# Performance work log

Measured on AMD Instinct MI355X. Metric: run time of the kernel, lower is better.

Reference implementation:

```python
import jax, jax.numpy as jnp
import numpy as np


def setup_inputs() -> dict:
    key = jax.random.key(0)
    k1, k2, k3 = jax.random.split(key, 3)
    B, N = 1024, 32768
    inputs = jax.random.normal(k1, (B, N), dtype=jnp.float32)
    targets = jax.random.randint(k2, (B,), 0, 16384, dtype=jnp.int64)
    postive_list = jax.random.randint(k3, (B,), 0, 64, dtype=jnp.int64)
    return {"inputs": inputs, "targets": targets, "postive_list": postive_list}


def reference(inputs, targets, postive_list):
    # log_softmax over the candidate axis
    logsm = jax.nn.log_softmax(inputs, axis=1)  # [B, N]
    N = inputs.shape[1]
    pos = jnp.arange(N)  # [N]
    start = targets[:, None]                      # [B, 1]
    end = (targets + postive_list)[:, None]       # inclusive end, [B, 1]
    mask = (pos[None, :] >= start) & (pos[None, :] <= end)  # [B, N]
    # per-sample mean of -log_softmax over the ragged range (length = postive+1)
    count = (postive_list + 1).astype(inputs.dtype)  # [B]
    per_sample = -jnp.sum(jnp.where(mask, logsm, 0.0), axis=1) / count  # [B]
    return jnp.mean(per_sample)
```

## Files before the change

kernel.cpp:

```cpp
#include <hip/hip_runtime.h>
#include <math.h>

#define THREADS 256
#define WAVES (THREADS / 64)

__global__ __launch_bounds__(THREADS)
void ce_loss_kernel(const float* __restrict__ x,
                    const int* __restrict__ targets,
                    const int* __restrict__ positives,
                    float* __restrict__ out,
                    int N, float invB)
{
    const int b = blockIdx.x;
    const float4* row4 = reinterpret_cast<const float4*>(x + (size_t)b * N);
    const int t0 = targets[b];
    const int t1 = t0 + positives[b];
    const int n4 = N >> 2;

    float m = -INFINITY;
    float s = 0.0f;
    float wsum = 0.0f;

    for (int i = threadIdx.x; i < n4; i += THREADS) {
        float4 v = row4[i];
        const int j = i << 2;

        float vm = fmaxf(fmaxf(v.x, v.y), fmaxf(v.z, v.w));
        if (vm > m) { s *= __expf(m - vm); m = vm; }
        s += __expf(v.x - m);
        s += __expf(v.y - m);
        s += __expf(v.z - m);
        s += __expf(v.w - m);

        wsum += (j     >= t0 && j     <= t1) ? v.x : 0.0f;
        wsum += (j + 1 >= t0 && j + 1 <= t1) ? v.y : 0.0f;
        wsum += (j + 2 >= t0 && j + 2 <= t1) ? v.z : 0.0f;
        wsum += (j + 3 >= t0 && j + 3 <= t1) ? v.w : 0.0f;
    }

    #pragma unroll
    for (int off = 32; off > 0; off >>= 1) {
        float om = __shfl_xor(m, off, 64);
        float os = __shfl_xor(s, off, 64);
        float ow = __shfl_xor(wsum, off, 64);
        float nm = fmaxf(m, om);
        s = s * __expf(m - nm) + os * __expf(om - nm);
        m = nm;
        wsum += ow;
    }

    __shared__ float sm[WAVES], ss[WAVES], sw[WAVES];
    const int wave = threadIdx.x >> 6;
    const int lane = threadIdx.x & 63;
    if (lane == 0) { sm[wave] = m; ss[wave] = s; sw[wave] = wsum; }
    __syncthreads();

    if (threadIdx.x == 0) {
        m = sm[0]; s = ss[0]; wsum = sw[0];
        #pragma unroll
        for (int w = 1; w < WAVES; ++w) {
            float om = sm[w], os = ss[w];
            float nm = fmaxf(m, om);
            s = s * __expf(m - nm) + os * __expf(om - nm);
            m = nm;
            wsum += sw[w];
        }
        const float count = (float)(t1 - t0 + 1);
        const float per_sample = (m + logf(s)) - wsum / count;
        atomicAdd(out, per_sample * invB);
    }
}

extern "C" void kernel_launch(void* const* d_in, const int* in_sizes, int n_in,
                              void* d_out, int out_size, void* d_ws, size_t ws_size,
                              hipStream_t stream) {
    const float* inputs    = (const float*)d_in[0];
    const int*   targets   = (const int*)d_in[1];
    const int*   positives = (const int*)d_in[2];
    float* out = (float*)d_out;

    const int B = in_sizes[1];
    const int N = in_sizes[0] / B;

    hipMemsetAsync(d_out, 0, sizeof(float), stream);

    ce_loss_kernel<<<B, THREADS, 0, stream>>>(inputs, targets, positives, out,
                                              N, 1.0f / (float)B);
}
```

Measured before the change: 201.9 us.

## Use multiple independent online-LSE accumulators, wider blocks, and two-stage final reduction

Each thread now keeps eight independent running max/sum pairs and processes two float4 loads per iteration, with 512 threads per block. This is meant to break the serial exp dependency chain and raise memory-level parallelism. The window check becomes a single unsigned compare. The atomic accumulation and memset are replaced by per-row results in the workspace plus a small reduction kernel. The per-element update now evaluates two exps instead of roughly one, and adds a second kernel launch.

```diff
diff --git a/kernel.cpp b/kernel.cpp
--- a/kernel.cpp
+++ b/kernel.cpp
@@ -1,74 +1,122 @@
 #include <hip/hip_runtime.h>
 #include <math.h>
 
-#define THREADS 256
+#define THREADS 512
 #define WAVES (THREADS / 64)
 
+#define LSE_UPD(mk, sk, v)                                    \
+    {                                                         \
+        float nm_ = fmaxf((mk), (v));                         \
+        (sk) = (sk) * __expf((mk) - nm_) + __expf((v) - nm_); \
+        (mk) = nm_;                                           \
+    }
+
+#define LSE_MERGE(ma, sa, mb, sb)                                  \
+    {                                                              \
+        float nm_ = fmaxf((ma), (mb));                             \
+        (sa) = (sa) * __expf((ma) - nm_) + (sb) * __expf((mb) - nm_); \
+        (ma) = nm_;                                                \
+    }
+
 __global__ __launch_bounds__(THREADS)
-void ce_loss_kernel(const float* __restrict__ x,
-                    const int* __restrict__ targets,
-                    const int* __restrict__ positives,
-                    float* __restrict__ out,
-                    int N, float invB)
+void ce_row_kernel(const float* __restrict__ x,
+                   const int* __restrict__ targets,
+                   const int* __restrict__ positives,
+                   float* __restrict__ row_out,
+                   int N)
 {
     const int b = blockIdx.x;
     const float4* row4 = reinterpret_cast<const float4*>(x + (size_t)b * N);
     const int t0 = targets[b];
-    const int t1 = t0 + positives[b];
+    const unsigned wlen = (unsigned)positives[b];
     const int n4 = N >> 2;
 
-    float m = -INFINITY;
-    float s = 0.0f;
-    float wsum = 0.0f;
+    float m0 = -INFINITY, m1 = -INFINITY, m2 = -INFINITY, m3 = -INFINITY;
+    float m4 = -INFINITY, m5 = -INFINITY, m6 = -INFINITY, m7 = -INFINITY;
+    float s0 = 0.f, s1 = 0.f, s2 = 0.f, s3 = 0.f;
+    float s4 = 0.f, s5 = 0.f, s6 = 0.f, s7 = 0.f;
+    float wsum = 0.f;
 
-    for (int i = threadIdx.x; i < n4; i += THREADS) {
-        float4 v = row4[i];
-        const int j = i << 2;
+    int i = threadIdx.x;
+    for (; i + THREADS < n4; i += 2 * THREADS) {
+        float4 a = row4[i];
+        float4 c = row4[i + THREADS];
+        const int ja = i << 2;
+        const int jc = (i + THREADS) << 2;
 
-        float vm = fmaxf(fmaxf(v.x, v.y), fmaxf(v.z, v.w));
-        if (vm > m) { s *= __expf(m - vm); m = vm; }
-        s += __expf(v.x - m);
-        s += __expf(v.y - m);
-        s += __expf(v.z - m);
-        s += __expf(v.w - m);
+        LSE_UPD(m0, s0, a.x); LSE_UPD(m1, s1, a.y);
+        LSE_UPD(m2, s2, a.z); LSE_UPD(m3, s3, a.w);
+        LSE_UPD(m4, s4, c.x); LSE_UPD(m5, s5, c.y);
+        LSE_UPD(m6, s6, c.z); LSE_UPD(m7, s7, c.w);
 
-        wsum += (j     >= t0 && j     <= t1) ? v.x : 0.0f;
-        wsum += (j + 1 >= t0 && j + 1 <= t1) ? v.y : 0.0f;
-        wsum += (j + 2 >= t0 && j + 2 <= t1) ? v.z : 0.0f;
-        wsum += (j + 3 >= t0 && j + 3 <= t1) ? v.w : 0.0f;
+        wsum += ((unsigned)(ja     - t0) <= wlen) ? a.x : 0.f;
+        wsum += ((unsigned)(ja + 1 - t0) <= wlen) ? a.y : 0.f;
+        wsum += ((unsigned)(ja + 2 - t0) <= wlen) ? a.z : 0.f;
+        wsum += ((unsigned)(ja + 3 - t0) <= wlen) ? a.w : 0.f;
+        wsum += ((unsigned)(jc     - t0) <= wlen) ? c.x : 0.f;
+        wsum += ((unsigned)(jc + 1 - t0) <= wlen) ? c.y : 0.f;
+        wsum += ((unsigned)(jc + 2 - t0) <= wlen) ? c.z : 0.f;
+        wsum += ((unsigned)(jc + 3 - t0) <= wlen) ? c.w : 0.f;
     }
+    if (i < n4) {
+        float4 a = row4[i];
+        const int ja = i << 2;
+        LSE_UPD(m0, s0, a.x); LSE_UPD(m1, s1, a.y);
+        LSE_UPD(m2, s2, a.z); LSE_UPD(m3, s3, a.w);
+        wsum += ((unsigned)(ja     - t0) <= wlen) ? a.x : 0.f;
+        wsum += ((unsigned)(ja + 1 - t0) <= wlen) ? a.y : 0.f;
+        wsum += ((unsigned)(ja + 2 - t0) <= wlen) ? a.z : 0.f;
+        wsum += ((unsigned)(ja + 3 - t0) <= wlen) ? a.w : 0.f;
+    }
+
+    LSE_MERGE(m0, s0, m1, s1); LSE_MERGE(m2, s2, m3, s3);
+    LSE_MERGE(m4, s4, m5, s5); LSE_MERGE(m6, s6, m7, s7);
+    LSE_MERGE(m0, s0, m2, s2); LSE_MERGE(m4, s4, m6, s6);
+    LSE_MERGE(m0, s0, m4, s4);
 
     #pragma unroll
     for (int off = 32; off > 0; off >>= 1) {
-        float om = __shfl_xor(m, off, 64);
-        float os = __shfl_xor(s, off, 64);
+        float om = __shfl_xor(m0, off, 64);
+        float os = __shfl_xor(s0, off, 64);
         float ow = __shfl_xor(wsum, off, 64);
-        float nm = fmaxf(m, om);
-        s = s * __expf(m - nm) + os * __expf(om - nm);
-        m = nm;
+        LSE_MERGE(m0, s0, om, os);
         wsum += ow;
     }
 
     __shared__ float sm[WAVES], ss[WAVES], sw[WAVES];
     const int wave = threadIdx.x >> 6;
     const int lane = threadIdx.x & 63;
-    if (lane == 0) { sm[wave] = m; ss[wave] = s; sw[wave] = wsum; }
+    if (lane == 0) { sm[wave] = m0; ss[wave] = s0; sw[wave] = wsum; }
     __syncthreads();
 
     if (threadIdx.x == 0) {
-        m = sm[0]; s = ss[0]; wsum = sw[0];
+        m0 = sm[0]; s0 = ss[0]; wsum = sw[0];
         #pragma unroll
         for (int w = 1; w < WAVES; ++w) {
-            float om = sm[w], os = ss[w];
-            float nm = fmaxf(m, om);
-            s = s * __expf(m - nm) + os * __expf(om - nm);
-            m = nm;
+            LSE_MERGE(m0, s0, sm[w], ss[w]);
             wsum += sw[w];
         }
-        const float count = (float)(t1 - t0 + 1);
-        const float per_sample = (m + logf(s)) - wsum / count;
-        atomicAdd(out, per_sample * invB);
+        const float count = (float)(wlen + 1u);
+        row_out[b] = (m0 + logf(s0)) - wsum / count;
     }
+}
+
+__global__ __launch_bounds__(256)
+void ce_reduce_kernel(const float* __restrict__ row_vals,
+                      float* __restrict__ out, int B, float invB)
+{
+    float acc = 0.f;
+    for (int i = threadIdx.x; i < B; i += 256) acc += row_vals[i];
+    #pragma unroll
+    for (int off = 32; off > 0; off >>= 1) acc += __shfl_xor(acc, off, 64);
+
+    __shared__ float sb[4];
+    const int wave = threadIdx.x >> 6;
+    const int lane = threadIdx.x & 63;
+    if (lane == 0) sb[wave] = acc;
+    __syncthreads();
+    if (threadIdx.x == 0)
+        out[0] = (sb[0] + sb[1] + sb[2] + sb[3]) * invB;
 }
 
 extern "C" void kernel_launch(void* const* d_in, const int* in_sizes, int n_in,
@@ -78,12 +126,12 @@
     const int*   targets   = (const int*)d_in[1];
     const int*   positives = (const int*)d_in[2];
     float* out = (float*)d_out;
+    float* row_vals = (float*)d_ws;
 
     const int B = in_sizes[1];
     const int N = in_sizes[0] / B;
 
-    hipMemsetAsync(d_out, 0, sizeof(float), stream);
-
-    ce_loss_kernel<<<B, THREADS, 0, stream>>>(inputs, targets, positives, out,
-                                              N, 1.0f / (float)B);
+    ce_row_kernel<<<B, THREADS, 0, stream>>>(inputs, targets, positives,
+                                             row_vals, N);
+    ce_reduce_kernel<<<1, 256, 0, stream>>>(row_vals, out, B, 1.0f / (float)B);
 }
```

After: 196.1 us. 2.8% less time.
